# Performance work log

Measured on AMD Instinct MI355X. Metric: run time of the kernel, lower is better.

Reference implementation:

```python
import jax, jax.numpy as jnp
import numpy as np

NUM_USER = 100000
NUM_ITEM = 50000
EMBED_DIM = 64
NUM_LAYER = 3
NUM_INTERACTIONS = 1600000  # symmetrized -> nnz = 3.2M
BATCH = 4096


def setup_inputs() -> dict:
    key = jax.random.key(0)
    k1, k2, k3, k4, k5, k6 = jax.random.split(key, 6)
    N = NUM_USER + NUM_ITEM
    user_emb = jax.random.normal(k1, (NUM_USER, EMBED_DIM), dtype=jnp.float32) / EMBED_DIM
    item_emb = jax.random.normal(k2, (NUM_ITEM, EMBED_DIM), dtype=jnp.float32) / EMBED_DIM
    # random bipartite interactions, symmetrized adjacency
    u = jax.random.randint(k3, (NUM_INTERACTIONS,), 0, NUM_USER, dtype=jnp.int32)
    i = jax.random.randint(k4, (NUM_INTERACTIONS,), 0, NUM_ITEM, dtype=jnp.int32) + NUM_USER
    adj_rows = jnp.concatenate([u, i])  # [nnz]
    adj_cols = jnp.concatenate([i, u])  # [nnz]
    # symmetric normalization D^-1/2 A D^-1/2
    deg = jax.ops.segment_sum(jnp.ones_like(adj_rows, dtype=jnp.float32), adj_rows, num_segments=N)
    deg = jnp.maximum(deg, 1.0)
    inv_sqrt = 1.0 / jnp.sqrt(deg)
    adj_vals = inv_sqrt[adj_rows] * inv_sqrt[adj_cols]
    user_ids = jax.random.randint(k5, (BATCH,), 0, NUM_USER, dtype=jnp.int32)
    item_ids = jax.random.randint(k6, (BATCH,), 0, NUM_ITEM, dtype=jnp.int32)
    return {"user_emb": user_emb, "item_emb": item_emb, "adj_vals": adj_vals,
            "adj_rows": adj_rows, "adj_cols": adj_cols,
            "user_ids": user_ids, "item_ids": item_ids}


def reference(user_emb, item_emb, adj_vals, adj_rows, adj_cols, user_ids, item_ids):
    num_user = user_emb.shape[0]
    N = num_user + item_emb.shape[0]
    x = jnp.concatenate([user_emb, item_emb], axis=0)  # [N, D]
    acc = x  # running sum == stack+mean over layers, fused
    for _ in range(NUM_LAYER):
        # SpMM: out[r] += vals * x[c]
        x = jax.ops.segment_sum(adj_vals[:, None] * x[adj_cols], adj_rows, num_segments=N)
        acc = acc + x
    emb = acc / (NUM_LAYER + 1)
    batch_user = emb[user_ids]                  # [B, D]
    batch_item = emb[num_user + item_ids]       # [B, D]
    scores = jnp.sum(batch_user * batch_item, axis=-1)  # DotProdScorer
    return scores
```

## Files before the change

kernel.cpp:

```cpp
#include <hip/hip_runtime.h>


#define DIM 64
#define TSHIFT 8
#define TMASK ((1 << TSHIFT) - 1)
#define TPAD 768
#define EWG 6272
#define STAGE_CAP 6272
#define NREP 4
#define RSTR 2560
#define TSTRIDE 10240

typedef unsigned short u16;
typedef unsigned char u8;
typedef unsigned int u32;

__device__ __forceinline__ u32 f2bf(float f) {
  u32 u = __float_as_uint(f);
  return (u + 0x7FFFu + ((u >> 16) & 1u)) >> 16;
}
__device__ __forceinline__ float bflo(u32 u) {
  return __uint_as_float(u << 16);
}
__device__ __forceinline__ float bfhi(u32 u) {
  return __uint_as_float(u & 0xFFFF0000u);
}

__device__ __forceinline__ int block_incl_scan(int lsum, int tid, int* wsum) {
  int lane = tid & 63, wv = tid >> 6;
  int v = lsum;
#pragma unroll
  for (int off = 1; off < 64; off <<= 1) {
    int t = __shfl_up(v, off, 64);
    if (lane >= off) v += t;
  }
  __syncthreads();
  if (lane == 63) wsum[wv] = v;
  __syncthreads();
  int add = 0;
  if (wv > 0) add += wsum[0];
  if (wv > 1) add += wsum[1];
  if (wv > 2) add += wsum[2];
  return v + add;
}


__global__ __launch_bounds__(256) void partition_direct(
    const int* __restrict__ rows, const int* __restrict__ cols, int nnz,
    int T, int* __restrict__ tcur, u32* __restrict__ bucket) {
  __shared__ u32 sorted[STAGE_CAP];
  __shared__ u16 sortedt[STAGE_CAP];
  __shared__ int cnt[TPAD], lstart[TPAD], gbase[TPAD];
  __shared__ int wsum[4];
  int w = blockIdx.x, tid = threadIdx.x;
  int rep = w & (NREP - 1);
  int j0 = tid * 3;
  cnt[j0] = 0; cnt[j0 + 1] = 0; cnt[j0 + 2] = 0;
  __syncthreads();
  int base = w * EWG;
  int end = min(base + EWG, nnz);
  int total = end - base;
  if (total <= 0) return;
  int nv = total >> 2;
  const int4* r4 = (const int4*)(rows + base);
  const int4* c4 = (const int4*)(cols + base);
  for (int i = tid; i < nv; i += 256) {
    int4 r = r4[i];
    atomicAdd(&cnt[r.x >> TSHIFT], 1);
    atomicAdd(&cnt[r.y >> TSHIFT], 1);
    atomicAdd(&cnt[r.z >> TSHIFT], 1);
    atomicAdd(&cnt[r.w >> TSHIFT], 1);
  }
  for (int e = base + (nv << 2) + tid; e < end; e += 256)
    atomicAdd(&cnt[rows[e] >> TSHIFT], 1);
  __syncthreads();
  int c0 = cnt[j0], c1 = cnt[j0 + 1], c2 = cnt[j0 + 2];
  int lsum = c0 + c1 + c2;
  int incl = block_incl_scan(lsum, tid, wsum);
  int excl = incl - lsum;
  lstart[j0] = excl;
  lstart[j0 + 1] = excl + c0;
  lstart[j0 + 2] = excl + c0 + c1;
  if (c0 > 0)
    gbase[j0] = j0 * TSTRIDE + rep * RSTR + atomicAdd(&tcur[j0 * NREP + rep], c0);
  if (c1 > 0)
    gbase[j0 + 1] = (j0 + 1) * TSTRIDE + rep * RSTR +
                    atomicAdd(&tcur[(j0 + 1) * NREP + rep], c1);
  if (c2 > 0)
    gbase[j0 + 2] = (j0 + 2) * TSTRIDE + rep * RSTR +
                    atomicAdd(&tcur[(j0 + 2) * NREP + rep], c2);
  cnt[j0] = 0; cnt[j0 + 1] = 0; cnt[j0 + 2] = 0;
  __syncthreads();
  for (int i = tid; i < nv; i += 256) {
    int4 r = r4[i];
    int4 c = c4[i];
    int t, s, d;
    t = r.x >> TSHIFT; s = atomicAdd(&cnt[t], 1); d = lstart[t] + s;
    sorted[d] = ((u32)(r.x & TMASK) << 18) | (u32)c.x; sortedt[d] = (u16)t;
    t = r.y >> TSHIFT; s = atomicAdd(&cnt[t], 1); d = lstart[t] + s;
    sorted[d] = ((u32)(r.y & TMASK) << 18) | (u32)c.y; sortedt[d] = (u16)t;
    t = r.z >> TSHIFT; s = atomicAdd(&cnt[t], 1); d = lstart[t] + s;
    sorted[d] = ((u32)(r.z & TMASK) << 18) | (u32)c.z; sortedt[d] = (u16)t;
    t = r.w >> TSHIFT; s = atomicAdd(&cnt[t], 1); d = lstart[t] + s;
    sorted[d] = ((u32)(r.w & TMASK) << 18) | (u32)c.w; sortedt[d] = (u16)t;
  }
  for (int e = base + (nv << 2) + tid; e < end; e += 256) {
    int r = rows[e];
    int c = cols[e];
    int t = r >> TSHIFT;
    int s = atomicAdd(&cnt[t], 1);
    int d = lstart[t] + s;
    sorted[d] = ((u32)(r & TMASK) << 18) | (u32)c;
    sortedt[d] = (u16)t;
  }
  __syncthreads();
  for (int i = tid; i < total; i += 256) {
    int t = sortedt[i];
    bucket[(size_t)gbase[t] + (i - lstart[t])] = sorted[i];
  }
}


__global__ __launch_bounds__(256) void build_csr_y0(
    const u32* __restrict__ bucket, const int* __restrict__ tcur, int T,
    int U, int N, const float4* __restrict__ ue, const float4* __restrict__ ie,
    int* __restrict__ row_ptr, u32* __restrict__ csr,
    uint4* __restrict__ y0b) {
  __shared__ int tl[TPAD];
  __shared__ int hist[256];
  __shared__ int cur[256];
  __shared__ int wsum[4];
  int b = blockIdx.x;
  int t = (b & 1) ? (T - 1 - (b >> 1)) : (b >> 1);
  int tid = threadIdx.x;
  int j0 = tid * 3;
  int v0 = 0, v1 = 0, v2 = 0;
  if (j0 < T) {
    int4 q = ((const int4*)tcur)[j0];
    v0 = q.x + q.y + q.z + q.w;
  }
  if (j0 + 1 < T) {
    int4 q = ((const int4*)tcur)[j0 + 1];
    v1 = q.x + q.y + q.z + q.w;
  }
  if (j0 + 2 < T) {
    int4 q = ((const int4*)tcur)[j0 + 2];
    v2 = q.x + q.y + q.z + q.w;
  }
  int lsum = v0 + v1 + v2;
  int incl0 = block_incl_scan(lsum, tid, wsum);
  int excl0 = incl0 - lsum;
  tl[j0] = excl0 + v0;
  tl[j0 + 1] = excl0 + v0 + v1;
  tl[j0 + 2] = excl0 + v0 + v1 + v2;
  hist[tid] = 0;
  __syncthreads();
  int tbase = (t == 0) ? 0 : tl[t - 1];
  int4 rl = ((const int4*)tcur)[t];
#pragma unroll
  for (int rep = 0; rep < NREP; ++rep) {
    int len = (rep == 0) ? rl.x : (rep == 1) ? rl.y : (rep == 2) ? rl.z : rl.w;
    int rs = t * TSTRIDE + rep * RSTR;
    const uint4* b4 = (const uint4*)(bucket + rs);
    int nv = len >> 2;
    for (int i = tid; i < nv; i += 256) {
      uint4 e = b4[i];
      atomicAdd(&hist[e.x >> 18], 1);
      atomicAdd(&hist[e.y >> 18], 1);
      atomicAdd(&hist[e.z >> 18], 1);
      atomicAdd(&hist[e.w >> 18], 1);
    }
    for (int i = rs + (nv << 2) + tid; i < rs + len; i += 256)
      atomicAdd(&hist[bucket[i] >> 18], 1);
  }
  __syncthreads();
  int h = hist[tid];
  int incl = block_incl_scan(h, tid, wsum);
  int r = (t << TSHIFT) + tid;
  if (r < N) row_ptr[r + 1] = tbase + incl;
  if (t == 0 && tid == 0) row_ptr[0] = 0;
  cur[tid] = tbase + incl - h;
  __syncthreads();
  for (int pass = 0; pass < 8; ++pass) {
    int lr = pass * 32 + (tid >> 3);
    int q = tid & 7;
    int row = (t << TSHIFT) + lr;
    if (row < N) {
      float invs = rsqrtf((float)max(hist[lr], 1));
      const float4* src = (row < U) ? (ue + (size_t)row * 16 + q * 2)
                                    : (ie + (size_t)(row - U) * 16 + q * 2);
      float4 a = src[0], bb = src[1];
      uint4 o;
      o.x = f2bf(a.x * invs) | (f2bf(a.y * invs) << 16);
      o.y = f2bf(a.z * invs) | (f2bf(a.w * invs) << 16);
      o.z = f2bf(bb.x * invs) | (f2bf(bb.y * invs) << 16);
      o.w = f2bf(bb.z * invs) | (f2bf(bb.w * invs) << 16);
      y0b[(size_t)row * 8 + q] = o;
    }
  }
#pragma unroll
  for (int rep = 0; rep < NREP; ++rep) {
    int len = (rep == 0) ? rl.x : (rep == 1) ? rl.y : (rep == 2) ? rl.z : rl.w;
    int rs = t * TSTRIDE + rep * RSTR;
    const uint4* b4 = (const uint4*)(bucket + rs);
    int nv = len >> 2;
    for (int i = tid; i < nv; i += 256) {
      uint4 e = b4[i];
      csr[atomicAdd(&cur[e.x >> 18], 1)] = e.x & 0x3FFFFu;
      csr[atomicAdd(&cur[e.y >> 18], 1)] = e.y & 0x3FFFFu;
      csr[atomicAdd(&cur[e.z >> 18], 1)] = e.z & 0x3FFFFu;
      csr[atomicAdd(&cur[e.w >> 18], 1)] = e.w & 0x3FFFFu;
    }
    for (int i = rs + (nv << 2) + tid; i < rs + len; i += 256) {
      u32 e = bucket[i];
      csr[atomicAdd(&cur[e >> 18], 1)] = e & 0x3FFFFu;
    }
  }
}


#define ACC8(G)                                                              \
  s0 += bflo(G.x); s1 += bfhi(G.x);                                          \
  s2 += bflo(G.y); s3 += bfhi(G.y);                                          \
  s4 += bflo(G.z); s5 += bfhi(G.z);                                          \
  s6 += bflo(G.w); s7 += bfhi(G.w);

__global__ __launch_bounds__(256) void spmm_sum(
    const int* __restrict__ row_ptr, const u32* __restrict__ csr,
    const u16* __restrict__ yin, u16* __restrict__ yout, int n) {
  if (blockIdx.x == 0 && threadIdx.x < 8)
    ((uint4*)(yout + (size_t)n * DIM))[threadIdx.x] = make_uint4(0, 0, 0, 0);
  int row = (blockIdx.x * 256 + threadIdx.x) >> 3;
  int q8 = threadIdx.x & 7;
  if (row >= n) return;
  int start = row_ptr[row];
  int end = row_ptr[row + 1];
  float s0 = 0.f, s1 = 0.f, s2 = 0.f, s3 = 0.f;
  float s4 = 0.f, s5 = 0.f, s6 = 0.f, s7 = 0.f;
  int k = start;
  for (; k + 8 <= end; k += 8) {
    u32 c0 = csr[k],     c1 = csr[k + 1], c2 = csr[k + 2], c3 = csr[k + 3];
    u32 c4 = csr[k + 4], c5 = csr[k + 5], c6 = csr[k + 6], c7 = csr[k + 7];
    uint4 g0 = ((const uint4*)(yin + (size_t)c0 * DIM))[q8];
    uint4 g1 = ((const uint4*)(yin + (size_t)c1 * DIM))[q8];
    uint4 g2 = ((const uint4*)(yin + (size_t)c2 * DIM))[q8];
    uint4 g3 = ((const uint4*)(yin + (size_t)c3 * DIM))[q8];
    uint4 g4 = ((const uint4*)(yin + (size_t)c4 * DIM))[q8];
    uint4 g5 = ((const uint4*)(yin + (size_t)c5 * DIM))[q8];
    uint4 g6 = ((const uint4*)(yin + (size_t)c6 * DIM))[q8];
    uint4 g7 = ((const uint4*)(yin + (size_t)c7 * DIM))[q8];
    ACC8(g0) ACC8(g1) ACC8(g2) ACC8(g3) ACC8(g4) ACC8(g5) ACC8(g6) ACC8(g7)
  }
  for (; k + 4 <= end; k += 4) {
    u32 c0 = csr[k], c1 = csr[k + 1], c2 = csr[k + 2], c3 = csr[k + 3];
    uint4 g0 = ((const uint4*)(yin + (size_t)c0 * DIM))[q8];
    uint4 g1 = ((const uint4*)(yin + (size_t)c1 * DIM))[q8];
    uint4 g2 = ((const uint4*)(yin + (size_t)c2 * DIM))[q8];
    uint4 g3 = ((const uint4*)(yin + (size_t)c3 * DIM))[q8];
    ACC8(g0) ACC8(g1) ACC8(g2) ACC8(g3)
  }
  for (; k < end; ++k) {
    u32 c0 = csr[k];
    uint4 g0 = ((const uint4*)(yin + (size_t)c0 * DIM))[q8];
    ACC8(g0)
  }
  float inv = 1.0f / (float)max(end - start, 1);
  uint4 o;
  o.x = f2bf(s0 * inv) | (f2bf(s1 * inv) << 16);
  o.y = f2bf(s2 * inv) | (f2bf(s3 * inv) << 16);
  o.z = f2bf(s4 * inv) | (f2bf(s5 * inv) << 16);
  o.w = f2bf(s6 * inv) | (f2bf(s7 * inv) << 16);
  ((uint4*)(yout + (size_t)row * DIM))[q8] = o;
}


__device__ __forceinline__ void gather8(
    const int* __restrict__ row_ptr, const u32* __restrict__ csr,
    const u16* __restrict__ y, int row, int s, int q8, int n, float* o) {
  int start = row_ptr[row];
  int end = row_ptr[row + 1];
  float s0 = 0.f, s1 = 0.f, s2 = 0.f, s3 = 0.f;
  float s4 = 0.f, s5 = 0.f, s6 = 0.f, s7 = 0.f;
  for (int k = start + s; k < end; k += 16) {
    int k2 = k + 8;
    bool ok2 = k2 < end;
    u32 c0 = csr[k];
    u32 c1 = ok2 ? csr[k2] : (u32)n;
    uint4 g0 = ((const uint4*)(y + (size_t)c0 * DIM))[q8];
    uint4 g1 = ((const uint4*)(y + (size_t)c1 * DIM))[q8];
    ACC8(g0) ACC8(g1)
  }
  for (int m = 8; m <= 32; m <<= 1) {
    s0 += __shfl_xor(s0, m, 64); s1 += __shfl_xor(s1, m, 64);
    s2 += __shfl_xor(s2, m, 64); s3 += __shfl_xor(s3, m, 64);
    s4 += __shfl_xor(s4, m, 64); s5 += __shfl_xor(s5, m, 64);
    s6 += __shfl_xor(s6, m, 64); s7 += __shfl_xor(s7, m, 64);
  }
  o[0] = s0; o[1] = s1; o[2] = s2; o[3] = s3;
  o[4] = s4; o[5] = s5; o[6] = s6; o[7] = s7;
}

__global__ __launch_bounds__(256) void spmm3_score(
    const int* __restrict__ row_ptr, const u32* __restrict__ csr,
    const float* __restrict__ ue, const float* __restrict__ ie,
    const u16* __restrict__ y1b, const u16* __restrict__ y2b,
    const int* __restrict__ user_ids, const int* __restrict__ item_ids,
    int U, int N, int batch, float* __restrict__ out) {
  int w = (blockIdx.x * 256 + threadIdx.x) >> 6;
  int lane = threadIdx.x & 63;
  if (w >= batch) return;
  int s = lane >> 3;
  int q8 = lane & 7;
  int u = user_ids[w];
  int iti = item_ids[w];
  int it = iti + U;
  float gu[8], gi[8];
  gather8(row_ptr, csr, y2b, u, s, q8, N, gu);
  gather8(row_ptr, csr, y2b, it, s, q8, N, gi);
  int du = row_ptr[u + 1] - row_ptr[u];
  int di = row_ptr[it + 1] - row_ptr[it];
  float su = sqrtf((float)max(du, 1)), ru = 1.0f / su;
  float si = sqrtf((float)max(di, 1)), ri = 1.0f / si;
  const float4* pu = (const float4*)(ue + (size_t)u * DIM) + q8 * 2;
  const float4* pi = (const float4*)(ie + (size_t)iti * DIM) + q8 * 2;
  float4 a0a = pu[0], a0b = pu[1];
  float4 b0a = pi[0], b0b = pi[1];
  uint4 y1u = ((const uint4*)(y1b + (size_t)u * DIM))[q8];
  uint4 y2u = ((const uint4*)(y2b + (size_t)u * DIM))[q8];
  uint4 y1i = ((const uint4*)(y1b + (size_t)it * DIM))[q8];
  uint4 y2i = ((const uint4*)(y2b + (size_t)it * DIM))[q8];
  float a[8], b[8];
  a[0] = a0a.x + su * (bflo(y1u.x) + bflo(y2u.x)) + ru * gu[0];
  a[1] = a0a.y + su * (bfhi(y1u.x) + bfhi(y2u.x)) + ru * gu[1];
  a[2] = a0a.z + su * (bflo(y1u.y) + bflo(y2u.y)) + ru * gu[2];
  a[3] = a0a.w + su * (bfhi(y1u.y) + bfhi(y2u.y)) + ru * gu[3];
  a[4] = a0b.x + su * (bflo(y1u.z) + bflo(y2u.z)) + ru * gu[4];
  a[5] = a0b.y + su * (bfhi(y1u.z) + bfhi(y2u.z)) + ru * gu[5];
  a[6] = a0b.z + su * (bflo(y1u.w) + bflo(y2u.w)) + ru * gu[6];
  a[7] = a0b.w + su * (bfhi(y1u.w) + bfhi(y2u.w)) + ru * gu[7];
  b[0] = b0a.x + si * (bflo(y1i.x) + bflo(y2i.x)) + ri * gi[0];
  b[1] = b0a.y + si * (bfhi(y1i.x) + bfhi(y2i.x)) + ri * gi[1];
  b[2] = b0a.z + si * (bflo(y1i.y) + bflo(y2i.y)) + ri * gi[2];
  b[3] = b0a.w + si * (bfhi(y1i.y) + bfhi(y2i.y)) + ri * gi[3];
  b[4] = b0b.x + si * (bflo(y1i.z) + bflo(y2i.z)) + ri * gi[4];
  b[5] = b0b.y + si * (bfhi(y1i.z) + bfhi(y2i.z)) + ri * gi[5];
  b[6] = b0b.z + si * (bflo(y1i.w) + bflo(y2i.w)) + ri * gi[6];
  b[7] = b0b.w + si * (bfhi(y1i.w) + bfhi(y2i.w)) + ri * gi[7];
  float p = 0.f;
  for (int j = 0; j < 8; ++j) p += a[j] * b[j];
  p += __shfl_xor(p, 1, 64);
  p += __shfl_xor(p, 2, 64);
  p += __shfl_xor(p, 4, 64);
  if (lane == 0) out[w] = p * (1.0f / 16.0f);
}

extern "C" void kernel_launch(void* const* d_in, const int* in_sizes, int n_in,
                              void* d_out, int out_size, void* d_ws, size_t ws_size,
                              hipStream_t stream) {
  const float* user_emb = (const float*)d_in[0];
  const float* item_emb = (const float*)d_in[1];
  const int* adj_rows = (const int*)d_in[3];
  const int* adj_cols = (const int*)d_in[4];
  const int* user_ids = (const int*)d_in[5];
  const int* item_ids = (const int*)d_in[6];
  float* scores = (float*)d_out;

  const int U = in_sizes[0] / DIM;
  const int I = in_sizes[1] / DIM;
  const int N = U + I;
  const int nnz = in_sizes[2];
  const int B = in_sizes[5];

  const int T = (N + TMASK) >> TSHIFT;
  const int npw = (nnz + EWG - 1) / EWG;

  char* p = (char*)d_ws;
  auto carve = [&](size_t bytes) {
    void* r = (void*)p;
    p += (bytes + 255) & ~(size_t)255;
    return r;
  };
  u16* y0b = (u16*)carve((size_t)(N + 1) * DIM * 2);
  u16* y1b = (u16*)carve((size_t)(N + 1) * DIM * 2);
  u16* y2b = (u16*)carve((size_t)(N + 1) * DIM * 2);
  int* row_ptr = (int*)carve((size_t)(N + 1) * 4);
  int* tcur = (int*)carve((size_t)T * NREP * 4);
  u32* bucket = (u32*)carve((size_t)(T + 1) * TSTRIDE * 4);
  u32* csr = (u32*)carve((size_t)nnz * 4);

  hipMemsetAsync(tcur, 0, (size_t)T * NREP * 4, stream);

  partition_direct<<<npw, 256, 0, stream>>>(adj_rows, adj_cols, nnz, T, tcur,
                                            bucket);

  build_csr_y0<<<T, 256, 0, stream>>>(bucket, tcur, T, U, N,
                                      (const float4*)user_emb,
                                      (const float4*)item_emb, row_ptr,
                                      csr, (uint4*)y0b);

  const int sblocks = (N * 8 + 255) / 256;
  spmm_sum<<<sblocks, 256, 0, stream>>>(row_ptr, csr, y0b, y1b, N);
  spmm_sum<<<sblocks, 256, 0, stream>>>(row_ptr, csr, y1b, y2b, N);

  spmm3_score<<<(B + 3) / 4, 256, 0, stream>>>(row_ptr, csr, user_emb,
                                               item_emb, y1b, y2b, user_ids,
                                               item_ids, U, N, B, scores);
}
```

Before: 270.1 us.

## Split SpMM rows into column halves processed in separate passes with nontemporal loads

The SpMM kernel's thread mapping changes so that each row's 64-dim embedding is split into two 32-column halves. Users' first halves run first, then users' second halves, then the same for items, with 4 threads per row-half. This shrinks the gathered working set per phase so more of the source embedding half stays resident in L2/MALL. CSR index loads and output stores become nontemporal to keep them from evicting gathered rows. The cost is that CSR indices and row pointers are read twice per row.

```diff
diff --git a/kernel.cpp b/kernel.cpp
--- a/kernel.cpp
+++ b/kernel.cpp
@@ -14,6 +14,7 @@
 typedef unsigned short u16;
 typedef unsigned char u8;
 typedef unsigned int u32;
+typedef unsigned int uv4 __attribute__((ext_vector_type(4)));
 
 __device__ __forceinline__ u32 f2bf(float f) {
   u32 u = __float_as_uint(f);
@@ -225,52 +226,75 @@
   s4 += bflo(G.z); s5 += bfhi(G.z);                                          \
   s6 += bflo(G.w); s7 += bfhi(G.w);
 
-__global__ __launch_bounds__(256) void spmm_sum(
+__global__ __launch_bounds__(256) void spmm_sum_split(
     const int* __restrict__ row_ptr, const u32* __restrict__ csr,
-    const u16* __restrict__ yin, u16* __restrict__ yout, int n) {
-  if (blockIdx.x == 0 && threadIdx.x < 8)
-    ((uint4*)(yout + (size_t)n * DIM))[threadIdx.x] = make_uint4(0, 0, 0, 0);
-  int row = (blockIdx.x * 256 + threadIdx.x) >> 3;
-  int q8 = threadIdx.x & 7;
-  if (row >= n) return;
+    const u16* __restrict__ yin, u16* __restrict__ yout, int U, int I,
+    int n) {
+  if (blockIdx.x == 0 && threadIdx.x < 8) {
+    uv4 z = 0;
+    ((uv4*)(yout + (size_t)n * DIM))[threadIdx.x] = z;
+  }
+  int g = blockIdx.x * 256 + threadIdx.x;
+  int UT = U << 2, IT = I << 2;
+  int row, q4;
+  if (g < UT) {
+    row = g >> 2; q4 = g & 3;
+  } else if (g < 2 * UT) {
+    int h = g - UT; row = h >> 2; q4 = 4 + (h & 3);
+  } else if (g < 2 * UT + IT) {
+    int h = g - 2 * UT; row = U + (h >> 2); q4 = h & 3;
+  } else if (g < 2 * (UT + IT)) {
+    int h = g - 2 * UT - IT; row = U + (h >> 2); q4 = 4 + (h & 3);
+  } else {
+    return;
+  }
   int start = row_ptr[row];
   int end = row_ptr[row + 1];
   float s0 = 0.f, s1 = 0.f, s2 = 0.f, s3 = 0.f;
   float s4 = 0.f, s5 = 0.f, s6 = 0.f, s7 = 0.f;
   int k = start;
   for (; k + 8 <= end; k += 8) {
-    u32 c0 = csr[k],     c1 = csr[k + 1], c2 = csr[k + 2], c3 = csr[k + 3];
-    u32 c4 = csr[k + 4], c5 = csr[k + 5], c6 = csr[k + 6], c7 = csr[k + 7];
-    uint4 g0 = ((const uint4*)(yin + (size_t)c0 * DIM))[q8];
-    uint4 g1 = ((const uint4*)(yin + (size_t)c1 * DIM))[q8];
-    uint4 g2 = ((const uint4*)(yin + (size_t)c2 * DIM))[q8];
-    uint4 g3 = ((const uint4*)(yin + (size_t)c3 * DIM))[q8];
-    uint4 g4 = ((const uint4*)(yin + (size_t)c4 * DIM))[q8];
-    uint4 g5 = ((const uint4*)(yin + (size_t)c5 * DIM))[q8];
-    uint4 g6 = ((const uint4*)(yin + (size_t)c6 * DIM))[q8];
-    uint4 g7 = ((const uint4*)(yin + (size_t)c7 * DIM))[q8];
+    u32 c0 = __builtin_nontemporal_load(csr + k);
+    u32 c1 = __builtin_nontemporal_load(csr + k + 1);
+    u32 c2 = __builtin_nontemporal_load(csr + k + 2);
+    u32 c3 = __builtin_nontemporal_load(csr + k + 3);
+    u32 c4 = __builtin_nontemporal_load(csr + k + 4);
+    u32 c5 = __builtin_nontemporal_load(csr + k + 5);
+    u32 c6 = __builtin_nontemporal_load(csr + k + 6);
+    u32 c7 = __builtin_nontemporal_load(csr + k + 7);
+    uv4 g0 = ((const uv4*)(yin + (size_t)c0 * DIM))[q4];
+    uv4 g1 = ((const uv4*)(yin + (size_t)c1 * DIM))[q4];
+    uv4 g2 = ((const uv4*)(yin + (size_t)c2 * DIM))[q4];
+    uv4 g3 = ((const uv4*)(yin + (size_t)c3 * DIM))[q4];
+    uv4 g4 = ((const uv4*)(yin + (size_t)c4 * DIM))[q4];
+    uv4 g5 = ((const uv4*)(yin + (size_t)c5 * DIM))[q4];
+    uv4 g6 = ((const uv4*)(yin + (size_t)c6 * DIM))[q4];
+    uv4 g7 = ((const uv4*)(yin + (size_t)c7 * DIM))[q4];
     ACC8(g0) ACC8(g1) ACC8(g2) ACC8(g3) ACC8(g4) ACC8(g5) ACC8(g6) ACC8(g7)
   }
   for (; k + 4 <= end; k += 4) {
-    u32 c0 = csr[k], c1 = csr[k + 1], c2 = csr[k + 2], c3 = csr[k + 3];
-    uint4 g0 = ((const uint4*)(yin + (size_t)c0 * DIM))[q8];
-    uint4 g1 = ((const uint4*)(yin + (size_t)c1 * DIM))[q8];
-    uint4 g2 = ((const uint4*)(yin + (size_t)c2 * DIM))[q8];
-    uint4 g3 = ((const uint4*)(yin + (size_t)c3 * DIM))[q8];
+    u32 c0 = __builtin_nontemporal_load(csr + k);
+    u32 c1 = __builtin_nontemporal_load(csr + k + 1);
+    u32 c2 = __builtin_nontemporal_load(csr + k + 2);
+    u32 c3 = __builtin_nontemporal_load(csr + k + 3);
+    uv4 g0 = ((const uv4*)(yin + (size_t)c0 * DIM))[q4];
+    uv4 g1 = ((const uv4*)(yin + (size_t)c1 * DIM))[q4];
+    uv4 g2 = ((const uv4*)(yin + (size_t)c2 * DIM))[q4];
+    uv4 g3 = ((const uv4*)(yin + (size_t)c3 * DIM))[q4];
     ACC8(g0) ACC8(g1) ACC8(g2) ACC8(g3)
   }
   for (; k < end; ++k) {
-    u32 c0 = csr[k];
-    uint4 g0 = ((const uint4*)(yin + (size_t)c0 * DIM))[q8];
+    u32 c0 = __builtin_nontemporal_load(csr + k);
+    uv4 g0 = ((const uv4*)(yin + (size_t)c0 * DIM))[q4];
     ACC8(g0)
   }
   float inv = 1.0f / (float)max(end - start, 1);
-  uint4 o;
+  uv4 o;
   o.x = f2bf(s0 * inv) | (f2bf(s1 * inv) << 16);
   o.y = f2bf(s2 * inv) | (f2bf(s3 * inv) << 16);
   o.z = f2bf(s4 * inv) | (f2bf(s5 * inv) << 16);
   o.w = f2bf(s6 * inv) | (f2bf(s7 * inv) << 16);
-  ((uint4*)(yout + (size_t)row * DIM))[q8] = o;
+  __builtin_nontemporal_store(o, (uv4*)(yout + (size_t)row * DIM) + q4);
 }
 
 
@@ -398,9 +422,12 @@
                                       (const float4*)item_emb, row_ptr,
                                       csr, (uint4*)y0b);
 
-  const int sblocks = (N * 8 + 255) / 256;
-  spmm_sum<<<sblocks, 256, 0, stream>>>(row_ptr, csr, y0b, y1b, N);
-  spmm_sum<<<sblocks, 256, 0, stream>>>(row_ptr, csr, y1b, y2b, N);
+  const int sthreads = (U + I) * 8;
+  const int sblocks = (sthreads + 255) / 256;
+  spmm_sum_split<<<sblocks, 256, 0, stream>>>(row_ptr, csr, y0b, y1b, U, I,
+                                              N);
+  spmm_sum_split<<<sblocks, 256, 0, stream>>>(row_ptr, csr, y1b, y2b, U, I,
+                                              N);
 
   spmm3_score<<<(B + 3) / 4, 256, 0, stream>>>(row_ptr, csr, user_emb,
                                                item_emb, y1b, y2b, user_ids,
```

Result: slower. 357.2 us (+32.3%).
